# Kernel optimization log

Measured on AMD Instinct MI355X. Metric: run time of the kernel, lower is better.

The kernel has to match this reference:

```python
import jax, jax.numpy as jnp
import numpy as np


def setup_inputs() -> dict:
    key = jax.random.key(0)
    k1, k2, k3 = jax.random.split(key, 3)
    B, H, S, D = 2, 8, 4096, 64
    queries = jax.random.normal(k1, (B, H, S, D), dtype=jnp.float32)
    keys = jax.random.normal(k2, (B, H, S, D), dtype=jnp.float32)
    values = jax.random.normal(k3, (B, H, S, D), dtype=jnp.float32)
    mask = jnp.zeros((1, 1, S, S), dtype=jnp.float32)
    return {"queries": queries, "keys": keys, "values": values, "d_k": D, "mask": mask}


def reference(queries, keys, values, d_k, mask):
    # scores: [B, H, Sq, Sk]
    scale = 1.0 / jnp.sqrt(jnp.asarray(d_k, dtype=queries.dtype))
    scores = jnp.einsum("bhqd,bhkd->bhqk", queries, keys) * scale
    scores = scores + (-1e9) * mask  # additive mask, broadcasts over B, H
    weights = jax.nn.softmax(scores, axis=-1)
    return jnp.einsum("bhqk,bhkd->bhqd", weights, values)
```

## Files before the change

kernel.cpp:

```cpp
#include <hip/hip_runtime.h>

#define S_LEN 4096
#define DHEAD 64
#define BK    64
#define NT    (S_LEN / BK)
#define TILE_HALFS (BK * DHEAD)

typedef __fp16   pk16x2 __attribute__((ext_vector_type(2)));
typedef _Float16 half8  __attribute__((ext_vector_type(8)));
typedef float    f32x16 __attribute__((ext_vector_type(16)));
typedef unsigned uint2v __attribute__((ext_vector_type(2)));

#define MFMA32(a, b, c) __builtin_amdgcn_mfma_f32_32x32x16_f16(a, b, c, 0, 0, 0)

__device__ __forceinline__ unsigned pk2u(float a, float b) {
    union { pk16x2 p; unsigned u; } x;
    x.p = __builtin_amdgcn_cvt_pkrtz(a, b);
    return x.u;
}

__device__ __forceinline__ uint2v pls(unsigned x, unsigned y) {
    return __builtin_amdgcn_permlane32_swap(x, y, false, false);
}
__device__ __forceinline__ float xmax32(float v) {
    uint2v r = pls(__float_as_uint(v), __float_as_uint(v));
    return fmaxf(__uint_as_float(r.x), __uint_as_float(r.y));
}
__device__ __forceinline__ float xadd32(float v) {
    uint2v r = pls(__float_as_uint(v), __float_as_uint(v));
    return __uint_as_float(r.x) + __uint_as_float(r.y);
}

__global__ void mask_flag_kernel(const float4* __restrict__ mask, int* __restrict__ flag) {
    const long stride = 2048L * 256;
    long i = (long)blockIdx.x * 256 + threadIdx.x;
    int nz = 0;
    #pragma unroll
    for (int it = 0; it < 8; ++it) {
        float4 a = mask[i + it * stride];
        nz |= (a.x != 0.f) | (a.y != 0.f) | (a.z != 0.f) | (a.w != 0.f);
    }
    if (__any(nz)) {
        if ((threadIdx.x & 63) == 0) atomicOr(flag, 1);
    }
}

__global__ __launch_bounds__(256, 2) void attn32s_kernel(
    const float* __restrict__ Q, const float* __restrict__ K,
    const float* __restrict__ V, const int* __restrict__ dkp,
    const float* __restrict__ mask, const int* __restrict__ maskflag,
    float* __restrict__ O)
{
    const int bid = blockIdx.x;
    const int L   = (bid & 7) * 64 + (bid >> 3);
    const int bh  = L >> 5;
    const int qt  = L & 31;

    const int tid  = threadIdx.x;
    const int w    = tid >> 6;
    const int lane = tid & 63;
    const int l31  = lane & 31;
    const int h    = lane >> 5;
    const int cx   = lane & 7;
    const int vkey = (l31 ^ (l31 >> 3)) & 7;

    const long gbase = (long)bh * S_LEN * DHEAD;
    const float* Qh = Q + gbase;
    const float* Kh = K + gbase;
    const float* Vh = V + gbase;

    const int q0 = qt * 128 + w * 32;
    const float csq  = rsqrtf((float)dkp[0]) * 1.44269504088896f;
    const float mfac = -1e9f * 1.44269504088896f;
    const bool use_mask = (maskflag[0] != 0);

    __shared__ __align__(16) _Float16 KT[2][TILE_HALFS];
    __shared__ __align__(16) _Float16 VT[2][TILE_HALFS];

    half8 qf[4];
    #pragma unroll
    for (int ks = 0; ks < 4; ++ks) {
        const float4* src = (const float4*)(Qh + (long)(q0 + l31) * DHEAD + ks * 16 + h * 8);
        float4 a = src[0], b = src[1];
        union { unsigned u[4]; half8 h8; } u;
        u.u[0] = pk2u(a.x * csq, a.y * csq);
        u.u[1] = pk2u(a.z * csq, a.w * csq);
        u.u[2] = pk2u(b.x * csq, b.y * csq);
        u.u[3] = pk2u(b.z * csq, b.w * csq);
        qf[ks] = u.h8;
    }

    const int kr  = tid >> 2;
    const int ks4 = tid & 3;
    const int vrp = tid >> 3;
    const int vdq = tid & 7;
    const float* Kb = Kh + (long)kr * DHEAD + ks4 * 16;
    const float* Vb = Vh + (long)(2 * vrp) * DHEAD + vdq * 8;
    const int kcol0 = (((2 * ks4)     ^ (kr & 7)) << 3);
    const int kcol1 = (((2 * ks4 + 1) ^ (kr & 7)) << 3);
    const int vd0   = vdq * 8;
    const int voct  = vrp >> 2;
    const int vlow  = (2 * vrp) & 7;

    float4 kf[4], vf[4];
    auto load_tile = [&](int kt) {
        const float4* kp  = (const float4*)(Kb + (long)kt * TILE_HALFS);
        kf[0] = kp[0]; kf[1] = kp[1]; kf[2] = kp[2]; kf[3] = kp[3];
        const float4* vp0 = (const float4*)(Vb + (long)kt * TILE_HALFS);
        const float4* vp1 = (const float4*)(Vb + (long)kt * TILE_HALFS + DHEAD);
        vf[0] = vp0[0]; vf[1] = vp0[1]; vf[2] = vp1[0]; vf[3] = vp1[1];
    };
    auto store_tile = [&](int bb) {
        union { unsigned u[4]; half8 h8; } u0, u1;
        u0.u[0] = pk2u(kf[0].x, kf[0].y);
        u0.u[1] = pk2u(kf[0].z, kf[0].w);
        u0.u[2] = pk2u(kf[1].x, kf[1].y);
        u0.u[3] = pk2u(kf[1].z, kf[1].w);
        u1.u[0] = pk2u(kf[2].x, kf[2].y);
        u1.u[1] = pk2u(kf[2].z, kf[2].w);
        u1.u[2] = pk2u(kf[3].x, kf[3].y);
        u1.u[3] = pk2u(kf[3].z, kf[3].w);
        *(half8*)&KT[bb][kr * 64 + kcol0] = u0.h8;
        *(half8*)&KT[bb][kr * 64 + kcol1] = u1.h8;
        _Float16* vt = &VT[bb][0];
        #define VCOL(j) ((((voct ^ (j) ^ vdq) & 7) << 3) + vlow)
        *(pk16x2*)&vt[(vd0 + 0) * 64 + VCOL(0)] = __builtin_amdgcn_cvt_pkrtz(vf[0].x, vf[2].x);
        *(pk16x2*)&vt[(vd0 + 1) * 64 + VCOL(1)] = __builtin_amdgcn_cvt_pkrtz(vf[0].y, vf[2].y);
        *(pk16x2*)&vt[(vd0 + 2) * 64 + VCOL(2)] = __builtin_amdgcn_cvt_pkrtz(vf[0].z, vf[2].z);
        *(pk16x2*)&vt[(vd0 + 3) * 64 + VCOL(3)] = __builtin_amdgcn_cvt_pkrtz(vf[0].w, vf[2].w);
        *(pk16x2*)&vt[(vd0 + 4) * 64 + VCOL(4)] = __builtin_amdgcn_cvt_pkrtz(vf[1].x, vf[3].x);
        *(pk16x2*)&vt[(vd0 + 5) * 64 + VCOL(5)] = __builtin_amdgcn_cvt_pkrtz(vf[1].y, vf[3].y);
        *(pk16x2*)&vt[(vd0 + 6) * 64 + VCOL(6)] = __builtin_amdgcn_cvt_pkrtz(vf[1].z, vf[3].z);
        *(pk16x2*)&vt[(vd0 + 7) * 64 + VCOL(7)] = __builtin_amdgcn_cvt_pkrtz(vf[1].w, vf[3].w);
        #undef VCOL
    };

    f32x16 o0 = {0.f,0.f,0.f,0.f,0.f,0.f,0.f,0.f,0.f,0.f,0.f,0.f,0.f,0.f,0.f,0.f};
    f32x16 o1 = o0;
    float m_i = -INFINITY;
    float l_i = 0.0f;

    load_tile(0);
    store_tile(0);
    __syncthreads();

    for (int kt = 0; kt < NT; ++kt) {
        const int b = kt & 1;
        if (kt + 1 < NT) load_tile(kt + 1);

        f32x16 s0 = {0.f,0.f,0.f,0.f,0.f,0.f,0.f,0.f,0.f,0.f,0.f,0.f,0.f,0.f,0.f,0.f};
        f32x16 s1 = s0;
        __builtin_amdgcn_s_setprio(1);
        #pragma unroll
        for (int ks = 0; ks < 4; ++ks) {
            const int off = (((2 * ks + h) ^ cx) << 3);
            half8 a0 = *(const half8*)&KT[b][(l31 << 6) + off];
            half8 a1 = *(const half8*)&KT[b][2048 + (l31 << 6) + off];
            s0 = MFMA32(a0, qf[ks], s0);
            s1 = MFMA32(a1, qf[ks], s1);
        }
        __builtin_amdgcn_s_setprio(0);

        if (kt + 1 < NT) store_tile(b ^ 1);

        if (use_mask) {
            const float* mrow = mask + (long)(q0 + l31) * S_LEN + kt * BK;
            #pragma unroll
            for (int r = 0; r < 16; ++r) {
                const int k = (r & 3) + ((r >> 2) << 3) + (h << 2);
                s0[r] += mfac * mrow[k];
                s1[r] += mfac * mrow[32 + k];
            }
        }

        {
            float tt[8];
            #pragma unroll
            for (int i = 0; i < 8; ++i)
                tt[i] = fmaxf(fmaxf(s0[2*i], s0[2*i+1]), fmaxf(s1[2*i], s1[2*i+1]));
            float mx = fmaxf(fmaxf(fmaxf(tt[0], tt[1]), fmaxf(tt[2], tt[3])),
                             fmaxf(fmaxf(tt[4], tt[5]), fmaxf(tt[6], tt[7])));
            mx = xmax32(mx);
            const bool need = __any(mx > m_i + 8.0f);
            const float mnew = need ? fmaxf(m_i, mx) : m_i;
            float ra = 0.f, rb = 0.f;
            #pragma unroll
            for (int r = 0; r < 16; ++r) {
                float p0 = __builtin_amdgcn_exp2f(s0[r] - mnew);
                float p1 = __builtin_amdgcn_exp2f(s1[r] - mnew);
                s0[r] = p0; s1[r] = p1;
                ra += p0; rb += p1;
            }
            float rsum = xadd32(ra + rb);
            if (need) {
                const float alpha = __builtin_amdgcn_exp2f(m_i - mnew);
                #pragma unroll
                for (int r = 0; r < 16; ++r) {
                    const int qr = (r & 3) + ((r >> 2) << 3) + (h << 2);
                    float a_r = __shfl(alpha, qr, 64);
                    o0[r] *= a_r; o1[r] *= a_r;
                }
                l_i = alpha * l_i + rsum;
                m_i = mnew;
            } else {
                l_i += rsum;
            }
        }

        unsigned wp[16];
        #pragma unroll
        for (int d = 0; d < 8; ++d) {
            wp[d]     = pk2u(s0[2*d], s0[2*d+1]);
            wp[8 + d] = pk2u(s1[2*d], s1[2*d+1]);
        }

        __builtin_amdgcn_s_setprio(1);
        #pragma unroll
        for (int si = 0; si < 4; ++si) {
            const int bs = (si >> 1) * 8 + (si & 1) * 4;
            uint2v r0 = pls(wp[bs + 0], wp[bs + 2]);
            uint2v r1 = pls(wp[bs + 1], wp[bs + 3]);
            union { unsigned u[4]; half8 h8; } pa;
            pa.u[0] = r0.x; pa.u[1] = r1.x; pa.u[2] = r0.y; pa.u[3] = r1.y;
            const int voff = (((2 * si + h) ^ vkey) << 3);
            half8 v0 = *(const half8*)&VT[b][(l31 << 6) + voff];
            half8 v1 = *(const half8*)&VT[b][2048 + (l31 << 6) + (voff ^ 32)];
            o0 = MFMA32(pa.h8, v0, o0);
            o1 = MFMA32(pa.h8, v1, o1);
        }
        __builtin_amdgcn_s_setprio(0);

        if (kt + 1 < NT) __syncthreads();
    }

    float* dst = O + gbase;
    #pragma unroll
    for (int r = 0; r < 16; ++r) {
        const int qr = (r & 3) + ((r >> 2) << 3) + (h << 2);
        float lq = __shfl(l_i, qr, 64);
        float inv = __builtin_amdgcn_rcpf(lq);
        const long row = (long)(q0 + qr) * DHEAD;
        dst[row + l31]      = o0[r] * inv;
        dst[row + 32 + l31] = o1[r] * inv;
    }
}

extern "C" void kernel_launch(void* const* d_in, const int* in_sizes, int n_in,
                              void* d_out, int out_size, void* d_ws, size_t ws_size,
                              hipStream_t stream) {
    const float* Q    = (const float*)d_in[0];
    const float* K    = (const float*)d_in[1];
    const float* V    = (const float*)d_in[2];
    const int*   dk   = (const int*)d_in[3];
    const float* mask = (const float*)d_in[4];
    float* out = (float*)d_out;
    int* flag = (int*)d_ws;

    (void)hipMemsetAsync(flag, 0, sizeof(int), stream);
    mask_flag_kernel<<<2048, 256, 0, stream>>>((const float4*)mask, flag);

    attn32s_kernel<<<512, 256, 0, stream>>>(Q, K, V, dk, mask, flag, out);
}
```

Baseline: 239.4 us.

## Process two key tiles per iteration with a 4-deep LDS ring buffer

Result: slower. 251.6 us (+5.1%).

```diff
diff --git a/kernel.cpp b/kernel.cpp
--- a/kernel.cpp
+++ b/kernel.cpp
@@ -45,7 +45,7 @@
     }
 }
 
-__global__ __launch_bounds__(256, 2) void attn32s_kernel(
+__global__ __launch_bounds__(256, 2) void attn32p_kernel(
     const float* __restrict__ Q, const float* __restrict__ K,
     const float* __restrict__ V, const int* __restrict__ dkp,
     const float* __restrict__ mask, const int* __restrict__ maskflag,
@@ -74,8 +74,8 @@
     const float mfac = -1e9f * 1.44269504088896f;
     const bool use_mask = (maskflag[0] != 0);
 
-    __shared__ __align__(16) _Float16 KT[2][TILE_HALFS];
-    __shared__ __align__(16) _Float16 VT[2][TILE_HALFS];
+    __shared__ __align__(16) _Float16 KT[4][TILE_HALFS];
+    __shared__ __align__(16) _Float16 VT[4][TILE_HALFS];
 
     half8 qf[4];
     #pragma unroll
@@ -135,33 +135,64 @@
         #undef VCOL
     };
 
+    auto qk = [&](int bb, f32x16& sa, f32x16& sb) {
+        __builtin_amdgcn_s_setprio(1);
+        #pragma unroll
+        for (int ks = 0; ks < 4; ++ks) {
+            const int off = (((2 * ks + h) ^ cx) << 3);
+            half8 a0 = *(const half8*)&KT[bb][(l31 << 6) + off];
+            half8 a1 = *(const half8*)&KT[bb][2048 + (l31 << 6) + off];
+            sa = MFMA32(a0, qf[ks], sa);
+            sb = MFMA32(a1, qf[ks], sb);
+        }
+        __builtin_amdgcn_s_setprio(0);
+    };
+
     f32x16 o0 = {0.f,0.f,0.f,0.f,0.f,0.f,0.f,0.f,0.f,0.f,0.f,0.f,0.f,0.f,0.f,0.f};
     f32x16 o1 = o0;
     float m_i = -INFINITY;
     float l_i = 0.0f;
 
-    load_tile(0);
-    store_tile(0);
-    __syncthreads();
-
-    for (int kt = 0; kt < NT; ++kt) {
-        const int b = kt & 1;
-        if (kt + 1 < NT) load_tile(kt + 1);
-
-        f32x16 s0 = {0.f,0.f,0.f,0.f,0.f,0.f,0.f,0.f,0.f,0.f,0.f,0.f,0.f,0.f,0.f,0.f};
-        f32x16 s1 = s0;
+    auto pv = [&](int bb, const f32x16& sa, const f32x16& sb) {
+        unsigned wp[16];
+        #pragma unroll
+        for (int d = 0; d < 8; ++d) {
+            wp[d]     = pk2u(sa[2*d], sa[2*d+1]);
+            wp[8 + d] = pk2u(sb[2*d], sb[2*d+1]);
+        }
         __builtin_amdgcn_s_setprio(1);
         #pragma unroll
-        for (int ks = 0; ks < 4; ++ks) {
-            const int off = (((2 * ks + h) ^ cx) << 3);
-            half8 a0 = *(const half8*)&KT[b][(l31 << 6) + off];
-            half8 a1 = *(const half8*)&KT[b][2048 + (l31 << 6) + off];
-            s0 = MFMA32(a0, qf[ks], s0);
-            s1 = MFMA32(a1, qf[ks], s1);
+        for (int si = 0; si < 4; ++si) {
+            const int bs = (si >> 1) * 8 + (si & 1) * 4;
+            uint2v r0 = pls(wp[bs + 0], wp[bs + 2]);
+            uint2v r1 = pls(wp[bs + 1], wp[bs + 3]);
+            union { unsigned u[4]; half8 h8; } pa;
+            pa.u[0] = r0.x; pa.u[1] = r1.x; pa.u[2] = r0.y; pa.u[3] = r1.y;
+            const int voff = (((2 * si + h) ^ vkey) << 3);
+            half8 v0 = *(const half8*)&VT[bb][(l31 << 6) + voff];
+            half8 v1 = *(const half8*)&VT[bb][2048 + (l31 << 6) + (voff ^ 32)];
+            o0 = MFMA32(pa.h8, v0, o0);
+            o1 = MFMA32(pa.h8, v1, o1);
         }
         __builtin_amdgcn_s_setprio(0);
-
-        if (kt + 1 < NT) store_tile(b ^ 1);
+    };
+
+    load_tile(0); store_tile(0);
+    load_tile(1); store_tile(1);
+    __syncthreads();
+
+    for (int kt = 0; kt < NT; kt += 2) {
+        const int b0 = kt & 3, b1 = (kt + 1) & 3;
+
+        if (kt + 2 < NT) load_tile(kt + 2);
+
+        f32x16 s0 = {0.f,0.f,0.f,0.f,0.f,0.f,0.f,0.f,0.f,0.f,0.f,0.f,0.f,0.f,0.f,0.f};
+        f32x16 s1 = s0, s2 = s0, s3 = s0;
+        qk(b0, s0, s1);
+        if (kt + 2 < NT) store_tile((kt + 2) & 3);
+
+        if (kt + 3 < NT) load_tile(kt + 3);
+        qk(b1, s2, s3);
 
         if (use_mask) {
             const float* mrow = mask + (long)(q0 + l31) * S_LEN + kt * BK;
@@ -170,14 +201,20 @@
                 const int k = (r & 3) + ((r >> 2) << 3) + (h << 2);
                 s0[r] += mfac * mrow[k];
                 s1[r] += mfac * mrow[32 + k];
+                s2[r] += mfac * mrow[BK + k];
+                s3[r] += mfac * mrow[BK + 32 + k];
             }
         }
 
         {
-            float tt[8];
-            #pragma unroll
-            for (int i = 0; i < 8; ++i)
-                tt[i] = fmaxf(fmaxf(s0[2*i], s0[2*i+1]), fmaxf(s1[2*i], s1[2*i+1]));
+            float tt[16];
+            #pragma unroll
+            for (int i = 0; i < 8; ++i) {
+                tt[i]     = fmaxf(fmaxf(s0[2*i], s0[2*i+1]), fmaxf(s1[2*i], s1[2*i+1]));
+                tt[8 + i] = fmaxf(fmaxf(s2[2*i], s2[2*i+1]), fmaxf(s3[2*i], s3[2*i+1]));
+            }
+            #pragma unroll
+            for (int i = 0; i < 8; ++i) tt[i] = fmaxf(tt[i], tt[8 + i]);
             float mx = fmaxf(fmaxf(fmaxf(tt[0], tt[1]), fmaxf(tt[2], tt[3])),
                              fmaxf(fmaxf(tt[4], tt[5]), fmaxf(tt[6], tt[7])));
             mx = xmax32(mx);
@@ -188,8 +225,10 @@
             for (int r = 0; r < 16; ++r) {
                 float p0 = __builtin_amdgcn_exp2f(s0[r] - mnew);
                 float p1 = __builtin_amdgcn_exp2f(s1[r] - mnew);
-                s0[r] = p0; s1[r] = p1;
-                ra += p0; rb += p1;
+                float p2 = __builtin_amdgcn_exp2f(s2[r] - mnew);
+                float p3 = __builtin_amdgcn_exp2f(s3[r] - mnew);
+                s0[r] = p0; s1[r] = p1; s2[r] = p2; s3[r] = p3;
+                ra += p0 + p1; rb += p2 + p3;
             }
             float rsum = xadd32(ra + rb);
             if (need) {
@@ -207,30 +246,12 @@
             }
         }
 
-        unsigned wp[16];
-        #pragma unroll
-        for (int d = 0; d < 8; ++d) {
-            wp[d]     = pk2u(s0[2*d], s0[2*d+1]);
-            wp[8 + d] = pk2u(s1[2*d], s1[2*d+1]);
-        }
-
-        __builtin_amdgcn_s_setprio(1);
-        #pragma unroll
-        for (int si = 0; si < 4; ++si) {
-            const int bs = (si >> 1) * 8 + (si & 1) * 4;
-            uint2v r0 = pls(wp[bs + 0], wp[bs + 2]);
-            uint2v r1 = pls(wp[bs + 1], wp[bs + 3]);
-            union { unsigned u[4]; half8 h8; } pa;
-            pa.u[0] = r0.x; pa.u[1] = r1.x; pa.u[2] = r0.y; pa.u[3] = r1.y;
-            const int voff = (((2 * si + h) ^ vkey) << 3);
-            half8 v0 = *(const half8*)&VT[b][(l31 << 6) + voff];
-            half8 v1 = *(const half8*)&VT[b][2048 + (l31 << 6) + (voff ^ 32)];
-            o0 = MFMA32(pa.h8, v0, o0);
-            o1 = MFMA32(pa.h8, v1, o1);
-        }
-        __builtin_amdgcn_s_setprio(0);
-
-        if (kt + 1 < NT) __syncthreads();
+        if (kt + 3 < NT) store_tile((kt + 3) & 3);
+
+        pv(b0, s0, s1);
+        pv(b1, s2, s3);
+
+        if (kt + 2 < NT) __syncthreads();
     }
 
     float* dst = O + gbase;
@@ -259,5 +280,5 @@
     (void)hipMemsetAsync(flag, 0, sizeof(int), stream);
     mask_flag_kernel<<<2048, 256, 0, stream>>>((const float4*)mask, flag);
 
-    attn32s_kernel<<<512, 256, 0, stream>>>(Q, K, V, dk, mask, flag, out);
-}
+    attn32p_kernel<<<512, 256, 0, stream>>>(Q, K, V, dk, mask, flag, out);
+}
```
